# Kernel tuning notes

Measured on AMD Instinct MI355X. Metric: run time of the kernel, lower is better.

Reference implementation:

```python
import jax, jax.numpy as jnp
import numpy as np

N_NODES = 500000
N_EDGES = 4000000
K = 4  # TAGConv hops


def _gcn_norm(edge_index, edge_weight, num_nodes):
    # PyG gcn_norm with add_self_loops=False (TAGConv default)
    src, dst = edge_index[0], edge_index[1]
    deg = jax.ops.segment_sum(edge_weight, dst, num_segments=num_nodes)
    dinv = jnp.where(deg > 0, jax.lax.rsqrt(deg), 0.0)
    return dinv[src] * edge_weight * dinv[dst]


def _tag_conv(x, src, dst, norm, Ws, b, num_nodes):
    # out = sum_{k=0..K} x_k @ Ws[k] + b,  x_k = hat(A) x_{k-1}
    out = x @ Ws[0]
    h = x
    for k in range(1, K + 1):
        msg = norm[:, None] * h[src]                      # [E, C]
        h = jax.ops.segment_sum(msg, dst, num_segments=num_nodes)
        out = out + h @ Ws[k]
    return out + b


def setup_inputs() -> dict:
    key = jax.random.key(0)
    ks = jax.random.split(key, 8)
    x = jax.random.normal(ks[0], (N_NODES, 2), dtype=jnp.float32)
    edge_index = jax.random.randint(ks[1], (2, N_EDGES), 0, N_NODES, dtype=jnp.int64)
    edge_weight = jax.random.uniform(ks[2], (N_EDGES,), dtype=jnp.float32)
    W1 = jax.random.normal(ks[3], (K + 1, 2, 16), dtype=jnp.float32) * 0.4
    b1 = jax.random.normal(ks[4], (16,), dtype=jnp.float32) * 0.1
    W2 = jax.random.normal(ks[5], (K + 1, 16, 16), dtype=jnp.float32) * 0.15
    b2 = jax.random.normal(ks[6], (16,), dtype=jnp.float32) * 0.1
    Wend = jax.random.normal(ks[7], (16, 1), dtype=jnp.float32) * 0.25
    return {"x": x, "edge_index": edge_index, "edge_weight": edge_weight,
            "W1": W1, "b1": b1, "W2": W2, "b2": b2, "Wend": Wend}


def reference(x, edge_index, edge_weight, W1, b1, W2, b2, Wend):
    src, dst = edge_index[0], edge_index[1]
    norm = _gcn_norm(edge_index, edge_weight, N_NODES)
    h = _tag_conv(x, src, dst, norm, W1, b1, N_NODES)      # conv1: 2 -> 16
    # num_layers=3 -> one relu+conv2 iteration
    h = jax.nn.relu(h)
    h = _tag_conv(h, src, dst, norm, W2, b2, N_NODES)      # conv2: 16 -> 16
    h = jax.nn.relu(h)
    y = h @ Wend                                           # endLinear (no bias)
    return jax.nn.sigmoid(y)                               # [N, 1]
```

## Files before the change

kernel.cpp:

```cpp
#include <hip/hip_runtime.h>
#include <hip/hip_fp16.h>
#include <math.h>


#define TB 256
#define TBLD 1024
#define TBIN 1024
#define BSHIFT 11
#define BW 2048
#define CAPB 17408
#define CAP 26624
#define HALF_CAP 13312
#define BIN_CHUNK 16384
#define WQ 8191.0f

typedef _Float16 half8 __attribute__((ext_vector_type(8)));
typedef float floatx4 __attribute__((ext_vector_type(4)));

__global__ __launch_bounds__(TBIN) void bin_kernel(
        const int* __restrict__ src, const int* __restrict__ dst,
        const float* __restrict__ w, int* __restrict__ binCount,
        uint2* __restrict__ binBuf, int E, int NB) {
    __shared__ int bcnt[256];
    __shared__ int bbase[256];
    for (int i = threadIdx.x; i < 256; i += TBIN) bcnt[i] = 0;
    __syncthreads();

    int base = blockIdx.x * BIN_CHUNK;
    int d[16];
#pragma unroll
    for (int j = 0; j < 16; j++) {
        int e = base + threadIdx.x + j * TBIN;
        d[j] = (e < E) ? dst[e] : -1;
        if (d[j] >= 0) atomicAdd(&bcnt[d[j] >> BSHIFT], 1);
    }
    __syncthreads();
    for (int i = threadIdx.x; i < NB; i += TBIN) {
        int c = bcnt[i];
        bbase[i] = c ? atomicAdd(&binCount[i], c) : 0;
        bcnt[i] = 0;
    }
    __syncthreads();
#pragma unroll
    for (int j = 0; j < 16; j++) {
        if (d[j] >= 0) {
            int e = base + threadIdx.x + j * TBIN;
            int b = d[j] >> BSHIFT;
            int off = bbase[b] + atomicAdd(&bcnt[b], 1);
            if (off < CAPB) {
                binBuf[(size_t)b * CAPB + off] =
                    make_uint2((unsigned)src[e] | ((unsigned)(d[j] & (BW - 1)) << 19),
                               __float_as_uint(w[e]));
            }
        }
    }
}

__global__ __launch_bounds__(TBLD) void build_kernel(
        const int* __restrict__ binCount, const uint2* __restrict__ binBuf,
        unsigned* __restrict__ payload, int* __restrict__ seg,
        float* __restrict__ dinv2, float* __restrict__ rdinv,
        const float* __restrict__ x, __half2* __restrict__ z0,
        int N, int NB) {
    __shared__ int   cnt[BW];
    __shared__ float wsum[BW];
    __shared__ int   start[BW];
    __shared__ unsigned short ord[HALF_CAP];
    __shared__ int   tmp[TBLD];
    __shared__ int   stot;
    int b = blockIdx.x;
    int nBase = b << BSHIFT;
    int nCount = min(BW, N - nBase);
    int m = min(binCount[b], CAPB);

    for (int i = threadIdx.x; i < BW; i += TBLD) { cnt[i] = 0; wsum[i] = 0.0f; }
    __syncthreads();

    const uint2* recs = binBuf + (size_t)b * CAPB;
    for (int i = threadIdx.x; i < m; i += TBLD) {
        uint2 r = recs[i];
        int ld = r.x >> 19;
        atomicAdd(&cnt[ld], 1);
        atomicAdd(&wsum[ld], __uint_as_float(r.y));
    }
    __syncthreads();

    int b2i = threadIdx.x * 2;
    int c0 = (cnt[b2i] + 7) & ~7;
    int c1 = (cnt[b2i + 1] + 7) & ~7;
    int s = c0 + c1;
    tmp[threadIdx.x] = s;
    __syncthreads();
    for (int off = 1; off < TBLD; off <<= 1) {
        int t = (threadIdx.x >= off) ? tmp[threadIdx.x - off] : 0;
        __syncthreads();
        tmp[threadIdx.x] += t;
        __syncthreads();
    }
    int run = tmp[threadIdx.x] - s;
    start[b2i] = run;
    start[b2i + 1] = run + c0;
    if (threadIdx.x == TBLD - 1) stot = run + s;
    __syncthreads();

    int tot = min(stot, CAP);
    int mid = (nCount > 1024) ? min(start[1024], CAP) : tot;

    for (int i = threadIdx.x; i < nCount; i += TBLD) {
        int n = nBase + i;
        int cc = cnt[i];
        int st = start[i];
        int ng = (cc + 7) >> 3;
        if (st >= CAP) { ng = 0; }
        else if (st + 8 * ng > CAP) { ng = (CAP - st) >> 3; }
        seg[n] = (st >> 3) | (ng << 16);
        float dsum = wsum[i];
        float di = (dsum > 0.0f) ? rsqrtf(dsum) : 0.0f;
        dinv2[n] = di * di;
        rdinv[n] = dsum * di;
        float2 xv = reinterpret_cast<const float2*>(x)[n];
        z0[n] = __float22half2_rn(make_float2(di * xv.x, di * xv.y));
    }
    __syncthreads();

    size_t pbase = (size_t)b * CAP;
    for (int half = 0; half < 2; half++) {
        int lo = half << 10, hi = lo + 1024;
        int pbeg = half ? mid : 0;
        int pend = half ? tot : mid;
        int limit = pend - pbeg;
        int limc = min(limit, HALF_CAP);

        for (int i = lo + threadIdx.x; i < hi; i += TBLD) cnt[i] = start[i] - pbeg;
        for (int j = threadIdx.x; j < limc; j += TBLD) ord[j] = 0xFFFF;
        __syncthreads();

        for (int i = threadIdx.x; i < m; i += TBLD) {
            uint2 r = recs[i];
            int ld = r.x >> 19;
            if (ld >= lo && ld < hi) {
                int pos = atomicAdd(&cnt[ld], 1);
                if ((unsigned)pos < (unsigned)limc) ord[pos] = (unsigned short)i;
            }
        }
        __syncthreads();

        for (int j = threadIdx.x; j < limc; j += TBLD) {
            unsigned short oi = ord[j];
            unsigned word = 0;
            if (oi != 0xFFFF) {
                uint2 r = recs[oi];
                unsigned q = (unsigned)__float2int_rn(__uint_as_float(r.y) * WQ);
                word = (r.x & 0x7FFFFu) | (q << 19);
            }
            payload[pbase + pbeg + j] = word;
        }
        for (int j = limc + threadIdx.x; j < limit; j += TBLD)
            payload[pbase + pbeg + j] = 0;
        __syncthreads();
    }
}


__device__ __forceinline__ void gacc2m(const unsigned* __restrict__ payload,
                                       const __half2* __restrict__ zin,
                                       int beg, int ng, float& ax, float& ay) {
    int g = 0;
    for (; g + 2 <= ng; g += 2, beg += 16) {
        uint4 r0 = *reinterpret_cast<const uint4*>(payload + beg);
        uint4 r1 = *reinterpret_cast<const uint4*>(payload + beg + 4);
        uint4 r2 = *reinterpret_cast<const uint4*>(payload + beg + 8);
        uint4 r3 = *reinterpret_cast<const uint4*>(payload + beg + 12);
        unsigned r[16] = {r0.x, r0.y, r0.z, r0.w, r1.x, r1.y, r1.z, r1.w,
                          r2.x, r2.y, r2.z, r2.w, r3.x, r3.y, r3.z, r3.w};
        __half2 v[16];
#pragma unroll
        for (int j = 0; j < 16; j++) v[j] = zin[r[j] & 0x7FFFFu];
#pragma unroll
        for (int j = 0; j < 16; j++) {
            float wv = (float)(r[j] >> 19) * (1.0f / WQ);
            float2 f = __half22float2(v[j]);
            ax += wv * f.x;
            ay += wv * f.y;
        }
    }
    if (g < ng) {
        uint4 r0 = *reinterpret_cast<const uint4*>(payload + beg);
        uint4 r1 = *reinterpret_cast<const uint4*>(payload + beg + 4);
        unsigned r[8] = {r0.x, r0.y, r0.z, r0.w, r1.x, r1.y, r1.z, r1.w};
        __half2 v[8];
#pragma unroll
        for (int j = 0; j < 8; j++) v[j] = zin[r[j] & 0x7FFFFu];
#pragma unroll
        for (int j = 0; j < 8; j++) {
            float wv = (float)(r[j] >> 19) * (1.0f / WQ);
            float2 f = __half22float2(v[j]);
            ax += wv * f.x;
            ay += wv * f.y;
        }
    }
}

__device__ __forceinline__ void gacc4(const unsigned* __restrict__ payload,
                                      const __half* __restrict__ ubase,
                                      int beg, int ng, float* __restrict__ h) {
    int g = 0;
    for (; g + 2 <= ng; g += 2, beg += 16) {
        uint4 r0 = *reinterpret_cast<const uint4*>(payload + beg);
        uint4 r1 = *reinterpret_cast<const uint4*>(payload + beg + 4);
        uint4 r2 = *reinterpret_cast<const uint4*>(payload + beg + 8);
        uint4 r3 = *reinterpret_cast<const uint4*>(payload + beg + 12);
        unsigned r[16] = {r0.x, r0.y, r0.z, r0.w, r1.x, r1.y, r1.z, r1.w,
                          r2.x, r2.y, r2.z, r2.w, r3.x, r3.y, r3.z, r3.w};
        float2 a[16];
#pragma unroll
        for (int j = 0; j < 16; j++)
            a[j] = *reinterpret_cast<const float2*>(ubase + 16LL * (int)(r[j] & 0x7FFFFu));
#pragma unroll
        for (int j = 0; j < 16; j++) {
            float wv = (float)(r[j] >> 19) * (1.0f / WQ);
            const __half2* hp = reinterpret_cast<const __half2*>(&a[j]);
            float2 v0 = __half22float2(hp[0]);
            float2 v1 = __half22float2(hp[1]);
            h[0] += wv * v0.x;
            h[1] += wv * v0.y;
            h[2] += wv * v1.x;
            h[3] += wv * v1.y;
        }
    }
    if (g < ng) {
        uint4 r0 = *reinterpret_cast<const uint4*>(payload + beg);
        uint4 r1 = *reinterpret_cast<const uint4*>(payload + beg + 4);
        unsigned r[8] = {r0.x, r0.y, r0.z, r0.w, r1.x, r1.y, r1.z, r1.w};
        float2 a[8];
#pragma unroll
        for (int j = 0; j < 8; j++)
            a[j] = *reinterpret_cast<const float2*>(ubase + 16LL * (int)(r[j] & 0x7FFFFu));
#pragma unroll
        for (int j = 0; j < 8; j++) {
            float wv = (float)(r[j] >> 19) * (1.0f / WQ);
            const __half2* hp = reinterpret_cast<const __half2*>(&a[j]);
            float2 v0 = __half22float2(hp[0]);
            float2 v1 = __half22float2(hp[1]);
            h[0] += wv * v0.x;
            h[1] += wv * v0.y;
            h[2] += wv * v1.x;
            h[3] += wv * v1.y;
        }
    }
}


__global__ void hop2_kernel(const int* __restrict__ seg, const unsigned* __restrict__ payload,
                            const __half2* __restrict__ zin, const float* __restrict__ dinv2,
                            __half2* __restrict__ zout, int N) {
    int n = blockIdx.x * TB + threadIdx.x;
    if (n >= N) return;
    int sp = seg[n];
    int beg = (n >> BSHIFT) * CAP + ((sp & 0xFFFF) << 3);
    int ng = sp >> 16;
    float ax = 0.0f, ay = 0.0f;
    gacc2m(payload, zin, beg, ng, ax, ay);
    float sc = dinv2[n];
    zout[n] = __float22half2_rn(make_float2(ax * sc, ay * sc));
}

__global__ void hop2_final_kernel(const int* __restrict__ seg, const unsigned* __restrict__ payload,
                                  const __half2* __restrict__ zbuf,
                                  const float* __restrict__ x,
                                  const float* __restrict__ rdinv, const float* __restrict__ dinv2,
                                  const float* __restrict__ W1, const float* __restrict__ b1,
                                  __half* __restrict__ g0, __half* __restrict__ u0, int N) {
    __shared__ float Ws[160];
    __shared__ float bs[16];
    for (int i = threadIdx.x; i < 160; i += blockDim.x) Ws[i] = W1[i];
    if (threadIdx.x < 16) bs[threadIdx.x] = b1[threadIdx.x];
    __syncthreads();

    int n = blockIdx.x * TB + threadIdx.x;
    if (n >= N) return;

    int sp = seg[n];
    int beg = (n >> BSHIFT) * CAP + ((sp & 0xFFFF) << 3);
    int ng = sp >> 16;
    const __half2* z3 = zbuf + (size_t)3 * N;
    float ax = 0.0f, ay = 0.0f;
    gacc2m(payload, z3, beg, ng, ax, ay);
    float sc = dinv2[n];
    float rd = rdinv[n];

    float coeff[10];
    {
        float2 v = reinterpret_cast<const float2*>(x)[n];
        coeff[0] = v.x; coeff[1] = v.y;
    }
#pragma unroll
    for (int k = 1; k <= 3; k++) {
        float2 v = __half22float2(zbuf[(size_t)k * N + n]);
        coeff[2 * k + 0] = rd * v.x;
        coeff[2 * k + 1] = rd * v.y;
    }
    coeff[8] = rd * sc * ax;
    coeff[9] = rd * sc * ay;

    float o[16];
#pragma unroll
    for (int c = 0; c < 16; c++) o[c] = bs[c];
#pragma unroll
    for (int j = 0; j < 10; j++) {
        float cf = coeff[j];
#pragma unroll
        for (int c = 0; c < 16; c++) o[c] += cf * Ws[j * 16 + c];
    }
#pragma unroll
    for (int c = 0; c < 16; c++) o[c] = fmaxf(o[c], 0.0f);

    float di = sc * rd;

    __half2 gp[8], up[8];
#pragma unroll
    for (int q = 0; q < 8; q++) {
        gp[q] = __float22half2_rn(make_float2(o[2 * q], o[2 * q + 1]));
        up[q] = __float22half2_rn(make_float2(di * o[2 * q], di * o[2 * q + 1]));
    }
    float4* gw = reinterpret_cast<float4*>(g0 + 16LL * n);
    gw[0] = *reinterpret_cast<float4*>(&gp[0]);
    gw[1] = *reinterpret_cast<float4*>(&gp[4]);
    float4* uw = reinterpret_cast<float4*>(u0 + 16LL * n);
    uw[0] = *reinterpret_cast<float4*>(&up[0]);
    uw[1] = *reinterpret_cast<float4*>(&up[4]);
}

__global__ void hop16_kernel(const int* __restrict__ seg, const unsigned* __restrict__ payload,
                             const __half* __restrict__ uin, const float* __restrict__ dinv2,
                             __half* __restrict__ uout, int N) {
    int gid = blockIdx.x * TB + threadIdx.x;
    int n = gid >> 2, quarter = gid & 3;
    if (n >= N) return;
    int sp = seg[n];
    int beg = (n >> BSHIFT) * CAP + ((sp & 0xFFFF) << 3);
    int ng = sp >> 16;

    float h[4] = {0.0f, 0.0f, 0.0f, 0.0f};
    gacc4(payload, uin + 4 * quarter, beg, ng, h);

    float sc = dinv2[n];
    __half2 p[2];
    p[0] = __float22half2_rn(make_float2(h[0] * sc, h[1] * sc));
    p[1] = __float22half2_rn(make_float2(h[2] * sc, h[3] * sc));
    *reinterpret_cast<float2*>(uout + 16LL * n + 4 * quarter) = *reinterpret_cast<float2*>(&p[0]);
}

__global__ void hop16_final_kernel(const int* __restrict__ seg, const unsigned* __restrict__ payload,
                                   const __half* __restrict__ g0, const __half* __restrict__ ubuf,
                                   const float* __restrict__ rdinv, const float* __restrict__ dinv2,
                                   const float* __restrict__ W2, const float* __restrict__ b2,
                                   const float* __restrict__ Wend, float* __restrict__ out, int N) {
    int lane = threadIdx.x & 63;
    int wave = threadIdx.x >> 6;
    int q = lane >> 4;
    int nn = lane & 15;
    int node_base = (blockIdx.x * 4 + wave) * 16;
    int node = node_base + nn;
    int nodec = min(node, N - 1);

    half8 bf[3];
#pragma unroll
    for (int t = 0; t < 3; t++) {
        half8 bv;
#pragma unroll
        for (int i = 0; i < 8; i++) {
            int K = 32 * t + 8 * q + i;
            K = (K < 80) ? K : 79;
            bv[i] = (_Float16)W2[K * 16 + nn];
        }
        bf[t] = bv;
    }
    float bsv = b2[nn];
    float wev = Wend[nn];

    int sp = seg[nodec];
    int beg = (nodec >> BSHIFT) * CAP + ((sp & 0xFFFF) << 3);
    int ng = sp >> 16;
    const __half* u3 = ubuf + (size_t)3 * 16 * N;
    float h[4] = {0.0f, 0.0f, 0.0f, 0.0f};
    gacc4(payload, u3 + 4 * q, beg, ng, h);

    float rd = rdinv[nodec];
    float sc = dinv2[nodec];

    const __half* a0p = ((q < 2) ? g0 : (ubuf + (size_t)16 * N)) + 16LL * nodec + 8 * (q & 1);
    half8 a0 = *reinterpret_cast<const half8*>(a0p);
    a0 = a0 * ((q >= 2) ? (_Float16)rd : (_Float16)1.0f);

    const __half* a1p = ((q < 2) ? (ubuf + (size_t)2 * 16 * N) : (ubuf + (size_t)3 * 16 * N))
                        + 16LL * nodec + 8 * (q & 1);
    half8 a1 = *reinterpret_cast<const half8*>(a1p);
    a1 = a1 * (_Float16)rd;

    float s4 = rd * sc;
    __half2 hh0 = __floats2half2_rn(h[0] * s4, h[1] * s4);
    __half2 hh1 = __floats2half2_rn(h[2] * s4, h[3] * s4);
    int p0, p1;
    p0 = *reinterpret_cast<int*>(&hh0);
    p1 = *reinterpret_cast<int*>(&hh1);
    int srcA = (nn + (q << 5)) & 63;
    int srcB = (srcA + 16) & 63;
    int lo0 = __shfl(p0, srcA, 64);
    int lo1 = __shfl(p1, srcA, 64);
    int hi0 = __shfl(p0, srcB, 64);
    int hi1 = __shfl(p1, srcB, 64);
    if (q >= 2) { lo0 = 0; lo1 = 0; hi0 = 0; hi1 = 0; }
    union { half8 v; int u[4]; } a2;
    a2.u[0] = lo0; a2.u[1] = lo1; a2.u[2] = hi0; a2.u[3] = hi1;

    floatx4 acc = {bsv, bsv, bsv, bsv};
    acc = __builtin_amdgcn_mfma_f32_16x16x32_f16(a0, bf[0], acc, 0, 0, 0);
    acc = __builtin_amdgcn_mfma_f32_16x16x32_f16(a1, bf[1], acc, 0, 0, 0);
    acc = __builtin_amdgcn_mfma_f32_16x16x32_f16(a2.v, bf[2], acc, 0, 0, 0);

    float svals[4];
#pragma unroll
    for (int r = 0; r < 4; r++) {
        float o = fmaxf(acc[r], 0.0f) * wev;
        o += __shfl_xor(o, 1, 64);
        o += __shfl_xor(o, 2, 64);
        o += __shfl_xor(o, 4, 64);
        o += __shfl_xor(o, 8, 64);
        svals[r] = o;
    }
    if (nn == 0) {
#pragma unroll
        for (int r = 0; r < 4; r++) {
            int on = node_base + q * 4 + r;
            if (on < N) out[on] = 1.0f / (1.0f + __expf(-svals[r]));
        }
    }
}

extern "C" void kernel_launch(void* const* d_in, const int* in_sizes, int n_in,
                              void* d_out, int out_size, void* d_ws, size_t ws_size,
                              hipStream_t stream) {
    const float* x    = (const float*)d_in[0];
    const int*   ei   = (const int*)d_in[1];
    const float* w    = (const float*)d_in[2];
    const float* W1   = (const float*)d_in[3];
    const float* b1   = (const float*)d_in[4];
    const float* W2   = (const float*)d_in[5];
    const float* b2   = (const float*)d_in[6];
    const float* Wend = (const float*)d_in[7];
    float* out = (float*)d_out;

    const int N = in_sizes[0] / 2;
    const int E = in_sizes[2];
    const int NB = (N + BW - 1) / BW;

    const int* src = ei;
    const int* dst = ei + E;

    int*      binCount = (int*)d_ws;
    unsigned* payload  = (unsigned*)(binCount + 1024);
    int*      seg      = (int*)(payload + (size_t)NB * CAP);
    float*    dinv2    = (float*)(seg + N);
    float*    rdinv    = dinv2 + N;
    __half2*  zbuf     = (__half2*)(rdinv + N);
    __half*   g0       = (__half*)(zbuf + (size_t)4 * N);
    __half*   ubuf     = g0 + (size_t)16 * N;
    uint2*    binBuf   = (uint2*)(ubuf + (size_t)16 * N);

    const int gE_bin = (E + BIN_CHUNK - 1) / BIN_CHUNK;
    const int gN   = (N + TB - 1) / TB;
    const int gN4  = (4 * N + TB - 1) / TB;
    const int gFin = (N + 63) / 64;

    hipMemsetAsync(binCount, 0, 1024 * sizeof(int), stream);

    bin_kernel<<<gE_bin, TBIN, 0, stream>>>(src, dst, w, binCount, binBuf, E, NB);
    build_kernel<<<NB, TBLD, 0, stream>>>(binCount, binBuf, payload, seg, dinv2, rdinv, x, zbuf, N, NB);

    for (int k = 1; k <= 3; k++) {
        hop2_kernel<<<gN, TB, 0, stream>>>(seg, payload, zbuf + (size_t)(k - 1) * N,
                                           dinv2, zbuf + (size_t)k * N, N);
    }
    hop2_final_kernel<<<gN, TB, 0, stream>>>(seg, payload, zbuf, x, rdinv, dinv2,
                                             W1, b1, g0, ubuf, N);

    for (int k = 1; k <= 3; k++) {
        hop16_kernel<<<gN4, TB, 0, stream>>>(seg, payload, ubuf + (size_t)(k - 1) * 16 * N,
                                             dinv2, ubuf + (size_t)k * 16 * N, N);
    }
    hop16_final_kernel<<<gFin, TB, 0, stream>>>(seg, payload, g0, ubuf, rdinv, dinv2,
                                                W2, b2, Wend, out, N);
}
```

Before: 544.7 us.

## Renumber nodes by degree bucket within each bin to balance per-thread gather work

Within each 2048-node bin, nodes are sorted into slots by their in-degree group count, so adjacent threads in a wavefront process nodes with similar edge counts and divergence drops. All per-node arrays (dinv2, rdinv, z0, seg, g0, ubuf) are stored in slot order, a new remap kernel rewrites payload source indices through an inverse map, and the final output is scattered back via an order array. This adds a pass over the payload, extra build work and scattered index lookups, and the ord buffer in shared memory is enlarged.

```diff
diff --git a/kernel.cpp b/kernel.cpp
--- a/kernel.cpp
+++ b/kernel.cpp
@@ -10,7 +10,7 @@
 #define BW 2048
 #define CAPB 17408
 #define CAP 26624
-#define HALF_CAP 13312
+#define HALF_CAP 20480
 #define BIN_CHUNK 16384
 #define WQ 8191.0f
 
@@ -60,13 +60,16 @@
         const int* __restrict__ binCount, const uint2* __restrict__ binBuf,
         unsigned* __restrict__ payload, int* __restrict__ seg,
         float* __restrict__ dinv2, float* __restrict__ rdinv,
+        int* __restrict__ order, int* __restrict__ inv,
         const float* __restrict__ x, __half2* __restrict__ z0,
         int N, int NB) {
     __shared__ int   cnt[BW];
     __shared__ float wsum[BW];
     __shared__ int   start[BW];
+    __shared__ unsigned short pos[BW];
     __shared__ unsigned short ord[HALF_CAP];
     __shared__ int   tmp[TBLD];
+    __shared__ int   hist[48];
     __shared__ int   stot;
     int b = blockIdx.x;
     int nBase = b << BSHIFT;
@@ -74,6 +77,7 @@
     int m = min(binCount[b], CAPB);
 
     for (int i = threadIdx.x; i < BW; i += TBLD) { cnt[i] = 0; wsum[i] = 0.0f; }
+    if (threadIdx.x < 48) hist[threadIdx.x] = 0;
     __syncthreads();
 
     const uint2* recs = binBuf + (size_t)b * CAPB;
@@ -85,11 +89,46 @@
     }
     __syncthreads();
 
+    for (int i = threadIdx.x; i < nCount; i += TBLD)
+        atomicAdd(&hist[min((cnt[i] + 7) >> 3, 15)], 1);
+    __syncthreads();
+    if (threadIdx.x == 0) {
+        int run = 0;
+        for (int j = 0; j < 16; j++) { hist[16 + j] = run; run += hist[j]; }
+    }
+    __syncthreads();
+    for (int i = threadIdx.x; i < nCount; i += TBLD) {
+        int k = min((cnt[i] + 7) >> 3, 15);
+        int p = hist[16 + k] + atomicAdd(&hist[32 + k], 1);
+        pos[i] = (unsigned short)p;
+        order[nBase + p] = nBase + i;
+        inv[nBase + i] = nBase + p;
+    }
+    __syncthreads();
+
+    for (int i = threadIdx.x; i < nCount; i += TBLD) {
+        int s = nBase + pos[i];
+        float dsum = wsum[i];
+        float di = (dsum > 0.0f) ? rsqrtf(dsum) : 0.0f;
+        dinv2[s] = di * di;
+        rdinv[s] = dsum * di;
+        float2 xv = reinterpret_cast<const float2*>(x)[nBase + i];
+        z0[s] = __float22half2_rn(make_float2(di * xv.x, di * xv.y));
+    }
+    __syncthreads();
+
+    int* scnt = (int*)wsum;
+    for (int s = threadIdx.x; s < BW; s += TBLD) scnt[s] = 0;
+    __syncthreads();
+    for (int i = threadIdx.x; i < nCount; i += TBLD)
+        scnt[pos[i]] = (cnt[i] + 7) & ~7;
+    __syncthreads();
+
     int b2i = threadIdx.x * 2;
-    int c0 = (cnt[b2i] + 7) & ~7;
-    int c1 = (cnt[b2i + 1] + 7) & ~7;
-    int s = c0 + c1;
-    tmp[threadIdx.x] = s;
+    int c0 = scnt[b2i];
+    int c1 = scnt[b2i + 1];
+    int ssum = c0 + c1;
+    tmp[threadIdx.x] = ssum;
     __syncthreads();
     for (int off = 1; off < TBLD; off <<= 1) {
         int t = (threadIdx.x >= off) ? tmp[threadIdx.x - off] : 0;
@@ -97,29 +136,23 @@
         tmp[threadIdx.x] += t;
         __syncthreads();
     }
-    int run = tmp[threadIdx.x] - s;
+    int run = tmp[threadIdx.x] - ssum;
     start[b2i] = run;
     start[b2i + 1] = run + c0;
-    if (threadIdx.x == TBLD - 1) stot = run + s;
+    if (threadIdx.x == TBLD - 1) stot = run + ssum;
     __syncthreads();
 
     int tot = min(stot, CAP);
     int mid = (nCount > 1024) ? min(start[1024], CAP) : tot;
 
     for (int i = threadIdx.x; i < nCount; i += TBLD) {
-        int n = nBase + i;
+        int p = pos[i];
+        int st = start[p];
         int cc = cnt[i];
-        int st = start[i];
         int ng = (cc + 7) >> 3;
         if (st >= CAP) { ng = 0; }
         else if (st + 8 * ng > CAP) { ng = (CAP - st) >> 3; }
-        seg[n] = (st >> 3) | (ng << 16);
-        float dsum = wsum[i];
-        float di = (dsum > 0.0f) ? rsqrtf(dsum) : 0.0f;
-        dinv2[n] = di * di;
-        rdinv[n] = dsum * di;
-        float2 xv = reinterpret_cast<const float2*>(x)[n];
-        z0[n] = __float22half2_rn(make_float2(di * xv.x, di * xv.y));
+        seg[nBase + p] = (st >> 3) | (ng << 16);
     }
     __syncthreads();
 
@@ -131,16 +164,17 @@
         int limit = pend - pbeg;
         int limc = min(limit, HALF_CAP);
 
-        for (int i = lo + threadIdx.x; i < hi; i += TBLD) cnt[i] = start[i] - pbeg;
+        for (int i = threadIdx.x; i < nCount; i += TBLD) cnt[i] = start[pos[i]] - pbeg;
         for (int j = threadIdx.x; j < limc; j += TBLD) ord[j] = 0xFFFF;
         __syncthreads();
 
         for (int i = threadIdx.x; i < m; i += TBLD) {
             uint2 r = recs[i];
             int ld = r.x >> 19;
-            if (ld >= lo && ld < hi) {
-                int pos = atomicAdd(&cnt[ld], 1);
-                if ((unsigned)pos < (unsigned)limc) ord[pos] = (unsigned short)i;
+            int sl = pos[ld];
+            if (sl >= lo && sl < hi) {
+                int p = atomicAdd(&cnt[ld], 1);
+                if ((unsigned)p < (unsigned)limc) ord[p] = (unsigned short)i;
             }
         }
         __syncthreads();
@@ -159,6 +193,18 @@
             payload[pbase + pbeg + j] = 0;
         __syncthreads();
     }
+}
+
+__global__ void remap_kernel(uint4* __restrict__ payload, const int* __restrict__ inv,
+                             int nquads, int N) {
+    int i = blockIdx.x * TB + threadIdx.x;
+    if (i >= nquads) return;
+    uint4 v = payload[i];
+    v.x = (v.x & ~0x7FFFFu) | (unsigned)inv[min((int)(v.x & 0x7FFFFu), N - 1)];
+    v.y = (v.y & ~0x7FFFFu) | (unsigned)inv[min((int)(v.y & 0x7FFFFu), N - 1)];
+    v.z = (v.z & ~0x7FFFFu) | (unsigned)inv[min((int)(v.z & 0x7FFFFu), N - 1)];
+    v.w = (v.w & ~0x7FFFFu) | (unsigned)inv[min((int)(v.w & 0x7FFFFu), N - 1)];
+    payload[i] = v;
 }
 
 
@@ -254,20 +300,20 @@
 __global__ void hop2_kernel(const int* __restrict__ seg, const unsigned* __restrict__ payload,
                             const __half2* __restrict__ zin, const float* __restrict__ dinv2,
                             __half2* __restrict__ zout, int N) {
-    int n = blockIdx.x * TB + threadIdx.x;
-    if (n >= N) return;
-    int sp = seg[n];
-    int beg = (n >> BSHIFT) * CAP + ((sp & 0xFFFF) << 3);
+    int s = blockIdx.x * TB + threadIdx.x;
+    if (s >= N) return;
+    int sp = seg[s];
+    int beg = (s >> BSHIFT) * CAP + ((sp & 0xFFFF) << 3);
     int ng = sp >> 16;
     float ax = 0.0f, ay = 0.0f;
     gacc2m(payload, zin, beg, ng, ax, ay);
-    float sc = dinv2[n];
-    zout[n] = __float22half2_rn(make_float2(ax * sc, ay * sc));
+    float sc = dinv2[s];
+    zout[s] = __float22half2_rn(make_float2(ax * sc, ay * sc));
 }
 
 __global__ void hop2_final_kernel(const int* __restrict__ seg, const unsigned* __restrict__ payload,
                                   const __half2* __restrict__ zbuf,
-                                  const float* __restrict__ x,
+                                  const float* __restrict__ x, const int* __restrict__ order,
                                   const float* __restrict__ rdinv, const float* __restrict__ dinv2,
                                   const float* __restrict__ W1, const float* __restrict__ b1,
                                   __half* __restrict__ g0, __half* __restrict__ u0, int N) {
@@ -277,26 +323,27 @@
     if (threadIdx.x < 16) bs[threadIdx.x] = b1[threadIdx.x];
     __syncthreads();
 
-    int n = blockIdx.x * TB + threadIdx.x;
-    if (n >= N) return;
-
-    int sp = seg[n];
-    int beg = (n >> BSHIFT) * CAP + ((sp & 0xFFFF) << 3);
+    int s = blockIdx.x * TB + threadIdx.x;
+    if (s >= N) return;
+
+    int sp = seg[s];
+    int beg = (s >> BSHIFT) * CAP + ((sp & 0xFFFF) << 3);
     int ng = sp >> 16;
     const __half2* z3 = zbuf + (size_t)3 * N;
     float ax = 0.0f, ay = 0.0f;
     gacc2m(payload, z3, beg, ng, ax, ay);
-    float sc = dinv2[n];
-    float rd = rdinv[n];
+    float sc = dinv2[s];
+    float rd = rdinv[s];
 
     float coeff[10];
     {
+        int n = order[s];
         float2 v = reinterpret_cast<const float2*>(x)[n];
         coeff[0] = v.x; coeff[1] = v.y;
     }
 #pragma unroll
     for (int k = 1; k <= 3; k++) {
-        float2 v = __half22float2(zbuf[(size_t)k * N + n]);
+        float2 v = __half22float2(zbuf[(size_t)k * N + s]);
         coeff[2 * k + 0] = rd * v.x;
         coeff[2 * k + 1] = rd * v.y;
     }
@@ -323,10 +370,10 @@
         gp[q] = __float22half2_rn(make_float2(o[2 * q], o[2 * q + 1]));
         up[q] = __float22half2_rn(make_float2(di * o[2 * q], di * o[2 * q + 1]));
     }
-    float4* gw = reinterpret_cast<float4*>(g0 + 16LL * n);
+    float4* gw = reinterpret_cast<float4*>(g0 + 16LL * s);
     gw[0] = *reinterpret_cast<float4*>(&gp[0]);
     gw[1] = *reinterpret_cast<float4*>(&gp[4]);
-    float4* uw = reinterpret_cast<float4*>(u0 + 16LL * n);
+    float4* uw = reinterpret_cast<float4*>(u0 + 16LL * s);
     uw[0] = *reinterpret_cast<float4*>(&up[0]);
     uw[1] = *reinterpret_cast<float4*>(&up[4]);
 }
@@ -335,24 +382,25 @@
                              const __half* __restrict__ uin, const float* __restrict__ dinv2,
                              __half* __restrict__ uout, int N) {
     int gid = blockIdx.x * TB + threadIdx.x;
-    int n = gid >> 2, quarter = gid & 3;
-    if (n >= N) return;
-    int sp = seg[n];
-    int beg = (n >> BSHIFT) * CAP + ((sp & 0xFFFF) << 3);
+    int s = gid >> 2, quarter = gid & 3;
+    if (s >= N) return;
+    int sp = seg[s];
+    int beg = (s >> BSHIFT) * CAP + ((sp & 0xFFFF) << 3);
     int ng = sp >> 16;
 
     float h[4] = {0.0f, 0.0f, 0.0f, 0.0f};
     gacc4(payload, uin + 4 * quarter, beg, ng, h);
 
-    float sc = dinv2[n];
+    float sc = dinv2[s];
     __half2 p[2];
     p[0] = __float22half2_rn(make_float2(h[0] * sc, h[1] * sc));
     p[1] = __float22half2_rn(make_float2(h[2] * sc, h[3] * sc));
-    *reinterpret_cast<float2*>(uout + 16LL * n + 4 * quarter) = *reinterpret_cast<float2*>(&p[0]);
+    *reinterpret_cast<float2*>(uout + 16LL * s + 4 * quarter) = *reinterpret_cast<float2*>(&p[0]);
 }
 
 __global__ void hop16_final_kernel(const int* __restrict__ seg, const unsigned* __restrict__ payload,
                                    const __half* __restrict__ g0, const __half* __restrict__ ubuf,
+                                   const int* __restrict__ order,
                                    const float* __restrict__ rdinv, const float* __restrict__ dinv2,
                                    const float* __restrict__ W2, const float* __restrict__ b2,
                                    const float* __restrict__ Wend, float* __restrict__ out, int N) {
@@ -360,9 +408,9 @@
     int wave = threadIdx.x >> 6;
     int q = lane >> 4;
     int nn = lane & 15;
-    int node_base = (blockIdx.x * 4 + wave) * 16;
-    int node = node_base + nn;
-    int nodec = min(node, N - 1);
+    int slot_base = (blockIdx.x * 4 + wave) * 16;
+    int slot = slot_base + nn;
+    int slotc = min(slot, N - 1);
 
     half8 bf[3];
 #pragma unroll
@@ -379,22 +427,22 @@
     float bsv = b2[nn];
     float wev = Wend[nn];
 
-    int sp = seg[nodec];
-    int beg = (nodec >> BSHIFT) * CAP + ((sp & 0xFFFF) << 3);
+    int sp = seg[slotc];
+    int beg = (slotc >> BSHIFT) * CAP + ((sp & 0xFFFF) << 3);
     int ng = sp >> 16;
     const __half* u3 = ubuf + (size_t)3 * 16 * N;
     float h[4] = {0.0f, 0.0f, 0.0f, 0.0f};
     gacc4(payload, u3 + 4 * q, beg, ng, h);
 
-    float rd = rdinv[nodec];
-    float sc = dinv2[nodec];
-
-    const __half* a0p = ((q < 2) ? g0 : (ubuf + (size_t)16 * N)) + 16LL * nodec + 8 * (q & 1);
+    float rd = rdinv[slotc];
+    float sc = dinv2[slotc];
+
+    const __half* a0p = ((q < 2) ? g0 : (ubuf + (size_t)16 * N)) + 16LL * slotc + 8 * (q & 1);
     half8 a0 = *reinterpret_cast<const half8*>(a0p);
     a0 = a0 * ((q >= 2) ? (_Float16)rd : (_Float16)1.0f);
 
     const __half* a1p = ((q < 2) ? (ubuf + (size_t)2 * 16 * N) : (ubuf + (size_t)3 * 16 * N))
-                        + 16LL * nodec + 8 * (q & 1);
+                        + 16LL * slotc + 8 * (q & 1);
     half8 a1 = *reinterpret_cast<const half8*>(a1p);
     a1 = a1 * (_Float16)rd;
 
@@ -432,8 +480,8 @@
     if (nn == 0) {
 #pragma unroll
         for (int r = 0; r < 4; r++) {
-            int on = node_base + q * 4 + r;
-            if (on < N) out[on] = 1.0f / (1.0f + __expf(-svals[r]));
+            int onS = slot_base + q * 4 + r;
+            if (onS < N) out[order[onS]] = 1.0f / (1.0f + __expf(-svals[r]));
         }
     }
 }
@@ -463,7 +511,9 @@
     int*      seg      = (int*)(payload + (size_t)NB * CAP);
     float*    dinv2    = (float*)(seg + N);
     float*    rdinv    = dinv2 + N;
-    __half2*  zbuf     = (__half2*)(rdinv + N);
+    int*      order    = (int*)(rdinv + N);
+    int*      inv      = order + N;
+    __half2*  zbuf     = (__half2*)(inv + N);
     __half*   g0       = (__half*)(zbuf + (size_t)4 * N);
     __half*   ubuf     = g0 + (size_t)16 * N;
     uint2*    binBuf   = (uint2*)(ubuf + (size_t)16 * N);
@@ -472,23 +522,27 @@
     const int gN   = (N + TB - 1) / TB;
     const int gN4  = (4 * N + TB - 1) / TB;
     const int gFin = (N + 63) / 64;
+    const int nquads = NB * (CAP / 4);
+    const int gRemap = (nquads + TB - 1) / TB;
 
     hipMemsetAsync(binCount, 0, 1024 * sizeof(int), stream);
 
     bin_kernel<<<gE_bin, TBIN, 0, stream>>>(src, dst, w, binCount, binBuf, E, NB);
-    build_kernel<<<NB, TBLD, 0, stream>>>(binCount, binBuf, payload, seg, dinv2, rdinv, x, zbuf, N, NB);
+    build_kernel<<<NB, TBLD, 0, stream>>>(binCount, binBuf, payload, seg, dinv2, rdinv,
+                                          order, inv, x, zbuf, N, NB);
+    remap_kernel<<<gRemap, TB, 0, stream>>>((uint4*)payload, inv, nquads, N);
 
     for (int k = 1; k <= 3; k++) {
         hop2_kernel<<<gN, TB, 0, stream>>>(seg, payload, zbuf + (size_t)(k - 1) * N,
                                            dinv2, zbuf + (size_t)k * N, N);
     }
-    hop2_final_kernel<<<gN, TB, 0, stream>>>(seg, payload, zbuf, x, rdinv, dinv2,
+    hop2_final_kernel<<<gN, TB, 0, stream>>>(seg, payload, zbuf, x, order, rdinv, dinv2,
                                              W1, b1, g0, ubuf, N);
 
     for (int k = 1; k <= 3; k++) {
         hop16_kernel<<<gN4, TB, 0, stream>>>(seg, payload, ubuf + (size_t)(k - 1) * 16 * N,
                                              dinv2, ubuf + (size_t)k * 16 * N, N);
     }
-    hop16_final_kernel<<<gFin, TB, 0, stream>>>(seg, payload, g0, ubuf, rdinv, dinv2,
+    hop16_final_kernel<<<gFin, TB, 0, stream>>>(seg, payload, g0, ubuf, order, rdinv, dinv2,
                                                 W2, b2, Wend, out, N);
 }
```

New measurement: 601.1 us. +10.3%, slower.
